# Optimization experiments

Hardware: AMD Instinct MI355X
Metric: run time of the kernel (lower is better)

## Reference

```python
import jax, jax.numpy as jnp
import numpy as np

D_MODEL = 512
N_HEADS = 8
MAX_DEPTH = 4
D_FF = 4 * D_MODEL
B, L = 4, 2048


def setup_inputs() -> dict:
    key = jax.random.key(0)
    ks = jax.random.split(key, 16)
    s = 0.02
    inp = {
        "x": jax.random.normal(ks[0], (B, L, D_MODEL), dtype=jnp.float32),
        # attention pre-norm
        "ln1_g": jnp.ones((D_MODEL,), jnp.float32),
        "ln1_b": jnp.zeros((D_MODEL,), jnp.float32),
        # MultiheadAttention in_proj (3D, D) and out_proj (D, D), torch (out, in) layout
        "Wqkv": jax.random.normal(ks[1], (3 * D_MODEL, D_MODEL), jnp.float32) * s,
        "bqkv": jnp.zeros((3 * D_MODEL,), jnp.float32),
        "Wo": jax.random.normal(ks[2], (D_MODEL, D_MODEL), jnp.float32) * s,
        "bo": jnp.zeros((D_MODEL,), jnp.float32),
        # FFN pre-norm + MLP
        "ln2_g": jnp.ones((D_MODEL,), jnp.float32),
        "ln2_b": jnp.zeros((D_MODEL,), jnp.float32),
        "W1": jax.random.normal(ks[3], (D_FF, D_MODEL), jnp.float32) * s,
        "b1": jnp.zeros((D_FF,), jnp.float32),
        "W2": jax.random.normal(ks[4], (D_MODEL, D_FF), jnp.float32) * s,
        "b2": jnp.zeros((D_MODEL,), jnp.float32),
        # token-choice depth router: LayerNorm + Linear(D,D) + GELU + Linear(D,max_depth)
        "rn_g": jnp.ones((D_MODEL,), jnp.float32),
        "rn_b": jnp.zeros((D_MODEL,), jnp.float32),
        "Rw1": jax.random.normal(ks[5], (D_MODEL, D_MODEL), jnp.float32) * s,
        "Rb1": jnp.zeros((D_MODEL,), jnp.float32),
        "Rw2": jax.random.normal(ks[6], (MAX_DEPTH, D_MODEL), jnp.float32) * s,
        "Rb2": jnp.zeros((MAX_DEPTH,), jnp.float32),
    }
    return inp


def _layernorm(x, g, b, eps=1e-5):
    mu = jnp.mean(x, axis=-1, keepdims=True)
    var = jnp.var(x, axis=-1, keepdims=True)
    return (x - mu) * jax.lax.rsqrt(var + eps) * g + b


def _block(x, ln1_g, ln1_b, Wqkv, bqkv, Wo, bo, ln2_g, ln2_b, W1, b1, W2, b2):
    Bb, Ll, D = x.shape
    H = N_HEADS
    dh = D // H
    # pre-norm self-attention
    h = _layernorm(x, ln1_g, ln1_b)
    qkv = h @ Wqkv.T + bqkv                      # (B, L, 3D)
    q, k, v = jnp.split(qkv, 3, axis=-1)
    q = q.reshape(Bb, Ll, H, dh)
    k = k.reshape(Bb, Ll, H, dh)
    v = v.reshape(Bb, Ll, H, dh)
    scores = jnp.einsum("blhd,bmhd->bhlm", q, k) / jnp.sqrt(jnp.float32(dh))
    attn = jax.nn.softmax(scores, axis=-1)
    o = jnp.einsum("bhlm,bmhd->blhd", attn, v).reshape(Bb, Ll, D)
    x = x + (o @ Wo.T + bo)
    # pre-norm FFN (exact-erf GELU, matching torch nn.GELU default)
    h2 = _layernorm(x, ln2_g, ln2_b)
    f = jax.nn.gelu(h2 @ W1.T + b1, approximate=False) @ W2.T + b2
    return x + f


def reference(x, ln1_g, ln1_b, Wqkv, bqkv, Wo, bo, ln2_g, ln2_b, W1, b1, W2, b2,
              rn_g, rn_b, Rw1, Rb1, Rw2, Rb2):
    # --- token-choice depth router (eval mode: argmax) ---
    rh = _layernorm(x, rn_g, rn_b)
    rh = jax.nn.gelu(rh @ Rw1.T + Rb1, approximate=False)
    router_logits = rh @ Rw2.T + Rb2             # (B, L, MAX_DEPTH)
    depths = jnp.argmax(router_logits, axis=-1) + 1  # (B, L) in [1, MAX_DEPTH]
    # --- dense recursion with torch.where-style selection ---
    cur = x
    for level in range(1, MAX_DEPTH + 1):
        upd = _block(cur, ln1_g, ln1_b, Wqkv, bqkv, Wo, bo,
                     ln2_g, ln2_b, W1, b1, W2, b2)
        keep = (depths >= level)[..., None]      # (B, L, 1)
        cur = jnp.where(keep, upd, cur)
    return cur, depths, router_logits
```

## Files before the change

kernel.cpp:

```cpp
#include <hip/hip_runtime.h>

typedef unsigned short u16;
typedef __attribute__((ext_vector_type(8))) short short8;
typedef __attribute__((ext_vector_type(4))) short s16x4;
typedef __attribute__((ext_vector_type(4))) float floatx4;
typedef __attribute__((ext_vector_type(4))) unsigned short u16x4;

#define NTOK 8192
#define DMODEL 512
#define DFF 2048
#define LSEQ 2048
#define RMARGIN 1e-3f

__device__ __forceinline__ u16 f2bf(float f) {
    union { float f; unsigned u; } x; x.f = f;
    unsigned r = (x.u + 0x7fffu + ((x.u >> 16) & 1u)) >> 16;
    return (u16)r;
}
__device__ __forceinline__ float bf2f(u16 h) {
    union { unsigned u; float f; } x; x.u = ((unsigned)h) << 16;
    return x.f;
}

__device__ __forceinline__ float geluf(float x) {
    return 0.5f * x * (1.0f + erff(x * 0.70710678118654752f));
}

__device__ __forceinline__ void gload_lds16(const void* g, void* l) {
    __builtin_amdgcn_global_load_lds(
        (const __attribute__((address_space(1))) void*)g,
        (__attribute__((address_space(3))) void*)l,
        16, 0, 0);
}

__device__ __forceinline__ s16x4 pack_p(float p0, float p1, float p2, float p3) {
    union { float f; unsigned u; } a{p0}, b{p1}, c{p2}, d{p3};
    union { unsigned u[2]; s16x4 s; } r;
    r.u[0] = (a.u >> 16) | (b.u & 0xffff0000u);
    r.u[1] = (c.u >> 16) | (d.u & 0xffff0000u);
    return r.s;
}

__global__ __launch_bounds__(256) void cvt_w(const float* __restrict__ wq,
                                             const float* __restrict__ wo,
                                             const float* __restrict__ w1,
                                             const float* __restrict__ w2,
                                             u16* __restrict__ out) {
    int i = blockIdx.x * 256 + threadIdx.x;
    float v;
    if (i < 786432)       v = wq[i];
    else if (i < 1048576) v = wo[i - 786432];
    else if (i < 2097152) v = w1[i - 1048576];
    else                  v = w2[i - 2097152];
    out[i] = f2bf(v);
}

__global__ __launch_bounds__(256) void copy_f32(const float* __restrict__ a,
                                                float* __restrict__ b) {
    size_t i = ((size_t)blockIdx.x * 256 + threadIdx.x) * 4;
    *(floatx4*)&b[i] = *(const floatx4*)&a[i];
}

__global__ __launch_bounds__(256) void cvt_rw1(const float* __restrict__ Rw1,
                                               u16* __restrict__ out) {
    const int i = blockIdx.x * 256 + threadIdx.x;
    const int n = i >> 9, k = i & 511;
    const float v = Rw1[i];
    const u16 hi = f2bf(v);
    const u16 lo = f2bf(v - bf2f(hi));
    out[(size_t)n * 1536 + k] = hi;
    out[(size_t)n * 1536 + 512 + k] = hi;
    out[(size_t)n * 1536 + 1024 + k] = lo;
}

__global__ __launch_bounds__(256) void cvt_split(const float* __restrict__ x,
                                                 u16* __restrict__ out,
                                                 int* __restrict__ cnt) {
    if (blockIdx.x == 0 && threadIdx.x == 0) *cnt = 0;
    const int i = blockIdx.x * 256 + threadIdx.x;
    const int base = i * 4;
    const int row = base >> 9, k = base & 511;
    const floatx4 v = *(const floatx4*)&x[base];
    u16x4 h, l;
#pragma unroll
    for (int e = 0; e < 4; ++e) {
        h[e] = f2bf(v[e]);
        l[e] = f2bf(v[e] - bf2f(h[e]));
    }
    u16* o = out + (size_t)row * 1536;
    *(u16x4*)&o[k] = h;
    *(u16x4*)&o[512 + k] = l;
    *(u16x4*)&o[1024 + k] = h;
}

__global__ __launch_bounds__(256)
void build_idx(const float* __restrict__ depthf, int* __restrict__ bcnt,
               int* __restrict__ idx) {
    __shared__ int sc[3][257];
    const int b = blockIdx.x;
    const int tid = threadIdx.x;
    const int t0 = (b << 11) + tid * 8;
    int dloc[8];
    int c2 = 0, c3 = 0, c4 = 0;
#pragma unroll
    for (int e = 0; e < 8; ++e) {
        dloc[e] = (int)depthf[t0 + e];
        c2 += (dloc[e] >= 2); c3 += (dloc[e] >= 3); c4 += (dloc[e] >= 4);
    }
    sc[0][tid + 1] = c2; sc[1][tid + 1] = c3; sc[2][tid + 1] = c4;
    if (tid == 0) { sc[0][0] = 0; sc[1][0] = 0; sc[2][0] = 0; }
    __syncthreads();
    for (int off = 1; off < 256; off <<= 1) {
        int v0 = 0, v1 = 0, v2 = 0;
        if (tid + 1 > off) {
            v0 = sc[0][tid + 1 - off];
            v1 = sc[1][tid + 1 - off];
            v2 = sc[2][tid + 1 - off];
        }
        __syncthreads();
        if (tid + 1 > off) {
            sc[0][tid + 1] += v0; sc[1][tid + 1] += v1; sc[2][tid + 1] += v2;
        }
        __syncthreads();
    }
    int p2 = sc[0][tid], p3 = sc[1][tid], p4 = sc[2][tid];
    const int seg = b << 11;
#pragma unroll
    for (int e = 0; e < 8; ++e) {
        const int t = t0 + e;
        idx[t] = t;
        if (dloc[e] >= 2) idx[8192 + seg + (p2++)] = t;
        if (dloc[e] >= 3) idx[16384 + seg + (p3++)] = t;
        if (dloc[e] >= 4) idx[24576 + seg + (p4++)] = t;
    }
    if (tid == 255) {
        bcnt[b]      = 2048;
        bcnt[4 + b]  = sc[0][256];
        bcnt[8 + b]  = sc[1][256];
        bcnt[12 + b] = sc[2][256];
    }
}

template<bool OUTF32, bool GATED>
__global__ __launch_bounds__(256)
void ln_k(const float* __restrict__ x, const float* __restrict__ g,
          const float* __restrict__ bb, void* __restrict__ outp,
          const int* __restrict__ bcnt) {
    const int row = blockIdx.x * 4 + (threadIdx.x >> 6);
    if (GATED) {
        if ((row & 2047) >= bcnt[row >> 11]) return;
    }
    const int lane = threadIdx.x & 63;
    const float* xr = x + (size_t)row * DMODEL;
    const int c0 = lane * 4, c1 = c0 + 256;
    floatx4 a = *(const floatx4*)&xr[c0];
    floatx4 b = *(const floatx4*)&xr[c1];
    float s = 0.f, sq = 0.f;
#pragma unroll
    for (int e = 0; e < 4; ++e) { s += a[e]; sq += a[e] * a[e]; }
#pragma unroll
    for (int e = 0; e < 4; ++e) { s += b[e]; sq += b[e] * b[e]; }
#pragma unroll
    for (int m = 32; m >= 1; m >>= 1) {
        s += __shfl_xor(s, m);
        sq += __shfl_xor(sq, m);
    }
    const float mean = s * (1.f / 512.f);
    const float rstd = rsqrtf(sq * (1.f / 512.f) - mean * mean + 1e-5f);
    floatx4 g0 = *(const floatx4*)&g[c0];
    floatx4 g1 = *(const floatx4*)&g[c1];
    floatx4 b0 = *(const floatx4*)&bb[c0];
    floatx4 b1 = *(const floatx4*)&bb[c1];
    floatx4 y0, y1;
#pragma unroll
    for (int e = 0; e < 4; ++e) {
        y0[e] = (a[e] - mean) * rstd * g0[e] + b0[e];
        y1[e] = (b[e] - mean) * rstd * g1[e] + b1[e];
    }
    if (OUTF32) {
        float* o = (float*)outp + (size_t)row * DMODEL;
        *(floatx4*)&o[c0] = y0;
        *(floatx4*)&o[c1] = y1;
    } else {
        u16* o = (u16*)outp + (size_t)row * DMODEL;
        u16x4 p0, p1;
#pragma unroll
        for (int e = 0; e < 4; ++e) { p0[e] = f2bf(y0[e]); p1[e] = f2bf(y1[e]); }
        *(u16x4*)&o[c0] = p0;
        *(u16x4*)&o[c1] = p1;
    }
}

template<int EPI, int BN>
__global__ __launch_bounds__(256, 2)
void gemm_bt(const u16* __restrict__ A, const u16* __restrict__ Bw,
             const float* __restrict__ bias,
             u16* __restrict__ Cb, float* __restrict__ Cf,
             const float* __restrict__ res,
             const int* __restrict__ IDX, const int* __restrict__ bcnt,
             u16* __restrict__ Cv,
             float aux, int N, int K) {
    constexpr int NJ = BN / 32;
    constexpr bool GATED = (EPI == 1 || EPI == 2 || EPI == 3);
    const int mBase = blockIdx.x * 128;
    int cntb = 0;
    if (GATED) {
        cntb = bcnt[mBase >> 11];
        if ((mBase & 2047) >= cntb) return;
    }
    __shared__ __align__(16) u16 As[128 * 32];
    __shared__ __align__(16) u16 Bs[BN * 32];
    const int tid = threadIdx.x;
    const int lane = tid & 63;
    const int w = tid >> 6;
    const int wm = (w >> 1) * 64;
    const int wn = (w & 1) * (BN / 2);
    const int nBase = blockIdx.y * BN;
    const int q4 = lane >> 4, rl = lane & 15;

    floatx4 acc[4][NJ];
#pragma unroll
    for (int i = 0; i < 4; ++i)
#pragma unroll
        for (int j = 0; j < NJ; ++j) acc[i][j] = (floatx4){0.f, 0.f, 0.f, 0.f};

    const int i0 = tid, i1 = tid + 256;
    const int ar0 = i0 >> 2, ac0 = ((i0 & 3) ^ ((i0 >> 3) & 3)) * 8;
    const int ar1 = i1 >> 2, ac1 = ((i1 & 3) ^ ((i1 >> 3) & 3)) * 8;
    const u16* pA0 = A + (size_t)(mBase + ar0) * K + ac0;
    const u16* pA1 = A + (size_t)(mBase + ar1) * K + ac1;
    const u16* pB0 = Bw + (size_t)(nBase + ar0) * K + ac0;
    const u16* pB1 = (BN == 128) ? Bw + (size_t)(nBase + ar1) * K + ac1 : pB0;
    u16* lA0 = &As[i0 * 8];
    u16* lA1 = &As[i1 * 8];
    u16* lB0 = &Bs[i0 * 8];
    u16* lB1 = (BN == 128) ? &Bs[i1 * 8] : lB0;

    for (int k0 = 0; k0 < K; k0 += 32) {
        gload_lds16(pA0, lA0);
        gload_lds16(pA1, lA1);
        gload_lds16(pB0, lB0);
        if (BN == 128) gload_lds16(pB1, lB1);
        pA0 += 32; pA1 += 32; pB0 += 32;
        if (BN == 128) pB1 += 32;
        __syncthreads();
        short8 af[4], bf[NJ];
#pragma unroll
        for (int t = 0; t < 4; ++t) {
            const int r = wm + t * 16 + rl;
            af[t] = *(const short8*)&As[r * 32 + (q4 ^ ((r >> 1) & 3)) * 8];
        }
#pragma unroll
        for (int t = 0; t < NJ; ++t) {
            const int r = wn + t * 16 + rl;
            bf[t] = *(const short8*)&Bs[r * 32 + (q4 ^ ((r >> 1) & 3)) * 8];
        }
#pragma unroll
        for (int ti = 0; ti < 4; ++ti)
#pragma unroll
            for (int tj = 0; tj < NJ; ++tj)
                acc[ti][tj] = __builtin_amdgcn_mfma_f32_16x16x32_bf16(
                    af[ti], bf[tj], acc[ti][tj], 0, 0, 0);
        __syncthreads();
    }

#pragma unroll
    for (int ti = 0; ti < 4; ++ti) {
        const int r0 = mBase + wm + ti * 16 + q4 * 4;
        int toks[4];
        if (EPI == 2 || EPI == 3) {
#pragma unroll
            for (int rr = 0; rr < 4; ++rr)
                toks[rr] = ((r0 + rr) & 2047) < cntb ? IDX[r0 + rr] : -1;
        }
#pragma unroll
        for (int tj = 0; tj < NJ; ++tj) {
            const int c = nBase + wn + tj * 16 + rl;
            const float bv = bias[c];
            if (EPI == 0) {
                if (nBase < 1024) {
                    const float sc = (nBase < 512) ? aux : 1.0f;
#pragma unroll
                    for (int rr = 0; rr < 4; ++rr)
                        Cb[(size_t)(r0 + rr) * 1024 + c] =
                            f2bf((acc[ti][tj][rr] + bv) * sc);
                } else {
                    const int cm = c - 1024;
                    const int hh = cm >> 6, dh = cm & 63;
                    const int bb2 = r0 >> 11, kv = r0 & 2047;
                    u16x4 pk;
#pragma unroll
                    for (int rr = 0; rr < 4; ++rr)
                        pk[rr] = f2bf(acc[ti][tj][rr] + bv);
                    *(u16x4*)&Cv[((size_t)(bb2 * 8 + hh) * 64 + dh) * 2048 + kv] = pk;
                }
            } else {
#pragma unroll
                for (int rr = 0; rr < 4; ++rr) {
                    const int r = r0 + rr;
                    const float v = acc[ti][tj][rr] + bv;
                    if (EPI == 1) {
                        Cb[(size_t)r * N + c] = f2bf(geluf(v));
                    } else if (EPI == 2) {
                        if (toks[rr] >= 0)
                            Cf[(size_t)r * N + c] =
                                res[(size_t)toks[rr] * N + c] + v;
                    } else if (EPI == 3) {
                        if (toks[rr] >= 0)
                            Cf[(size_t)toks[rr] * N + c] =
                                res[(size_t)r * N + c] + v;
                    } else {
                        Cf[(size_t)r * N + c] = geluf(v);
                    }
                }
            }
        }
    }
}

__global__ __launch_bounds__(256, 2)
void attn_k(const u16* __restrict__ qk, const u16* __restrict__ vT,
            u16* __restrict__ o, const int* __restrict__ IDX,
            const int* __restrict__ bcnt) {
    const int qt = blockIdx.x;
    const int bh = blockIdx.y;
    const int b = bh >> 3, h = bh & 7;
    const int cnt = bcnt[b];
    if (qt * 128 >= cnt) return;
    const int tid = threadIdx.x, lane = tid & 63, w = tid >> 6;
    const int tok0 = b * LSEQ;
    const int seg = b << 11;
    const int q4 = lane >> 4, rl = lane & 15;

    __shared__ __align__(16) u16 Kt[128 * 64];
    __shared__ __align__(16) u16 Vt[64 * 128];

    const u16* vbase = vT + (size_t)bh * 64 * 2048;

    const int pos0 = qt * 128 + w * 32 + rl;
    const int pos1 = pos0 + 16;
    const int tA = (pos0 < cnt) ? IDX[seg + pos0] : tok0;
    const int tB = (pos1 < cnt) ? IDX[seg + pos1] : tok0;

    short8 qf[2][2];
#pragma unroll
    for (int ks = 0; ks < 2; ++ks) {
        qf[0][ks] = *(const short8*)&qk[(size_t)tA * 1024 + h * 64 + ks * 32 + q4 * 8];
        qf[1][ks] = *(const short8*)&qk[(size_t)tB * 1024 + h * 64 + ks * 32 + q4 * 8];
    }

    floatx4 oacc[4][2];
#pragma unroll
    for (int dt = 0; dt < 4; ++dt)
#pragma unroll
        for (int nt = 0; nt < 2; ++nt) oacc[dt][nt] = (floatx4){0.f, 0.f, 0.f, 0.f};
    float lsum[2] = {0.f, 0.f};

    const u16* kp0 = &Kt[rl * 64 + ((q4 ^ (rl & 7))) * 8];
    const u16* kp1 = &Kt[rl * 64 + (((4 + q4) ^ (rl & 7))) * 8];

    for (int kt = 0; kt < 16; ++kt) {
        const int kv0 = kt * 128;
        __syncthreads();
#pragma unroll
        for (int it = 0; it < 4; ++it) {
            const int i = it * 256 + tid;
            const int r = i >> 3;
            const int c = ((i & 7) ^ (r & 7)) * 8;
            gload_lds16(&qk[(size_t)(tok0 + kv0 + r) * 1024 + 512 + h * 64 + c],
                        &Kt[i * 8]);
        }
#pragma unroll
        for (int it = 0; it < 4; ++it) {
            const int i = it * 256 + tid;
            const int dh = i >> 4;
            const int ch = (i & 15) ^ (dh & 15);
            gload_lds16(&vbase[(size_t)dh * 2048 + kv0 + ch * 8], &Vt[i * 8]);
        }
        __syncthreads();

#pragma unroll
        for (int mt = 0; mt < 8; ++mt) {
            const short8 kf0 = *(const short8*)&kp0[mt * 1024];
            const short8 kf1 = *(const short8*)&kp1[mt * 1024];
            floatx4 s[2];
#pragma unroll
            for (int nt = 0; nt < 2; ++nt) {
                s[nt] = __builtin_amdgcn_mfma_f32_16x16x32_bf16(kf0, qf[nt][0],
                        (floatx4){0.f, 0.f, 0.f, 0.f}, 0, 0, 0);
                s[nt] = __builtin_amdgcn_mfma_f32_16x16x32_bf16(kf1, qf[nt][1],
                        s[nt], 0, 0, 0);
            }
            s16x4 pb[2];
#pragma unroll
            for (int nt = 0; nt < 2; ++nt) {
                const float p0 = exp2f(s[nt][0]);
                const float p1 = exp2f(s[nt][1]);
                const float p2 = exp2f(s[nt][2]);
                const float p3 = exp2f(s[nt][3]);
                lsum[nt] += (p0 + p1) + (p2 + p3);
                pb[nt] = pack_p(p0, p1, p2, p3);
            }
            const int ct = 2 * mt + (q4 >> 1);
            const u16* vp = &Vt[(ct ^ rl) * 8 + (q4 & 1) * 4 + rl * 128];
#pragma unroll
            for (int dt = 0; dt < 4; ++dt) {
                const s16x4 vf = *(const s16x4*)&vp[dt * 2048];
#pragma unroll
                for (int nt = 0; nt < 2; ++nt)
                    oacc[dt][nt] = __builtin_amdgcn_mfma_f32_16x16x16bf16_1k(
                        vf, pb[nt], oacc[dt][nt], 0, 0, 0);
            }
        }
    }

#pragma unroll
    for (int nt = 0; nt < 2; ++nt) {
        float l = lsum[nt];
        l += __shfl_xor(l, 16);
        l += __shfl_xor(l, 32);
        const float inv = 1.0f / l;
        const int pos = (nt == 0) ? pos0 : pos1;
        if (pos < cnt) {
            const size_t row = seg + pos;
#pragma unroll
            for (int dt = 0; dt < 4; ++dt) {
                u16x4 pk;
#pragma unroll
                for (int rr = 0; rr < 4; ++rr) pk[rr] = f2bf(oacc[dt][nt][rr] * inv);
                *(u16x4*)&o[row * DMODEL + h * 64 + dt * 16 + q4 * 4] = pk;
            }
        }
    }
}

__global__ __launch_bounds__(256)
void router_logits_f32(const float* __restrict__ rr, const float* __restrict__ Rw2,
                       const float* __restrict__ Rb2, float* __restrict__ logits,
                       float* __restrict__ depthf, int* __restrict__ cnt,
                       int* __restrict__ list) {
    const int t = blockIdx.x * 4 + (threadIdx.x >> 6);
    const int lane = threadIdx.x & 63;
    const float* xr = rr + (size_t)t * 512;
    const int c0 = lane * 4, c1 = c0 + 256;
    floatx4 a = *(const floatx4*)&xr[c0];
    floatx4 b = *(const floatx4*)&xr[c1];
    float s[4];
#pragma unroll
    for (int d = 0; d < 4; ++d) {
        const float* wr = Rw2 + d * 512;
        floatx4 wa = *(const floatx4*)&wr[c0];
        floatx4 wb = *(const floatx4*)&wr[c1];
        float acc = 0.f;
#pragma unroll
        for (int e = 0; e < 4; ++e) acc += a[e] * wa[e];
#pragma unroll
        for (int e = 0; e < 4; ++e) acc += b[e] * wb[e];
        s[d] = acc;
    }
#pragma unroll
    for (int m = 32; m >= 1; m >>= 1)
#pragma unroll
        for (int d = 0; d < 4; ++d) s[d] += __shfl_xor(s[d], m);
    if (lane == 0) {
        float v[4];
        float bv = -1e30f; int best = 0;
#pragma unroll
        for (int d = 0; d < 4; ++d) {
            v[d] = s[d] + Rb2[d];
            logits[(size_t)t * 4 + d] = v[d];
            if (v[d] > bv) { bv = v[d]; best = d; }
        }
        float second = -1e30f;
#pragma unroll
        for (int d = 0; d < 4; ++d)
            if (d != best) second = fmaxf(second, v[d]);
        depthf[t] = (float)(best + 1);
        if (bv - second < RMARGIN) {
            int idx = atomicAdd(cnt, 1);
            list[idx] = t;
        }
    }
}

__global__ __launch_bounds__(256)
void router_exact(const float* __restrict__ rh, const float* __restrict__ Rw1,
                  const float* __restrict__ Rb1, const float* __restrict__ Rw2,
                  const float* __restrict__ Rb2, const int* __restrict__ cnt,
                  const int* __restrict__ list, float* __restrict__ logits,
                  float* __restrict__ depthf) {
    __shared__ float rhs[512];
    __shared__ double rrd[512];
    __shared__ double lg[4];
    const int n = *cnt;
    const int tid = threadIdx.x;
    for (int ii = blockIdx.x; ii < n; ii += gridDim.x) {
        const int t = list[ii];
        rhs[tid] = rh[(size_t)t * 512 + tid];
        rhs[tid + 256] = rh[(size_t)t * 512 + 256 + tid];
        __syncthreads();
#pragma unroll
        for (int oo = 0; oo < 2; ++oo) {
            const int nn = tid + oo * 256;
            double acc = (double)Rb1[nn];
            const float* wrow = Rw1 + (size_t)nn * 512;
            for (int k = 0; k < 512; ++k)
                acc = fma((double)rhs[k], (double)wrow[k], acc);
            rrd[nn] = 0.5 * acc * (1.0 + erf(acc * 0.70710678118654752440));
        }
        __syncthreads();
        const int w = tid >> 6, lane = tid & 63;
        double acc2 = 0.0;
        for (int k = lane; k < 512; k += 64)
            acc2 += rrd[k] * (double)Rw2[w * 512 + k];
#pragma unroll
        for (int m = 32; m >= 1; m >>= 1) acc2 += __shfl_xor(acc2, m);
        if (lane == 0) lg[w] = acc2 + (double)Rb2[w];
        __syncthreads();
        if (tid == 0) {
            double bv = -1e300; int best = 0;
#pragma unroll
            for (int d = 0; d < 4; ++d) {
                const double v = lg[d];
                logits[(size_t)t * 4 + d] = (float)v;
                if (v > bv) { bv = v; best = d; }
            }
            depthf[t] = (float)(best + 1);
        }
        __syncthreads();
    }
}

extern "C" void kernel_launch(void* const* d_in, const int* in_sizes, int n_in,
                              void* d_out, int out_size, void* d_ws, size_t ws_size,
                              hipStream_t stream) {
    (void)in_sizes; (void)n_in; (void)out_size; (void)ws_size;
    const float* x    = (const float*)d_in[0];
    const float* ln1g = (const float*)d_in[1];
    const float* ln1b = (const float*)d_in[2];
    const float* Wqkv = (const float*)d_in[3];
    const float* bqkv = (const float*)d_in[4];
    const float* Wo   = (const float*)d_in[5];
    const float* bo   = (const float*)d_in[6];
    const float* ln2g = (const float*)d_in[7];
    const float* ln2b = (const float*)d_in[8];
    const float* W1   = (const float*)d_in[9];
    const float* b1   = (const float*)d_in[10];
    const float* W2   = (const float*)d_in[11];
    const float* b2   = (const float*)d_in[12];
    const float* rng  = (const float*)d_in[13];
    const float* rnb  = (const float*)d_in[14];
    const float* Rw1  = (const float*)d_in[15];
    const float* Rb1  = (const float*)d_in[16];
    const float* Rw2  = (const float*)d_in[17];
    const float* Rb2  = (const float*)d_in[18];

    float* cur    = (float*)d_out;
    float* depthf = cur + (size_t)NTOK * DMODEL;
    float* logits = depthf + NTOK;

    char* ws = (char*)d_ws;
    float* xmid = (float*)ws;
    u16* sbuf   = (u16*)(ws + 16777216);
    u16* qk     = (u16*)(ws + 25165824);
    u16* ffb    = (u16*)(ws + 41943040);
    u16* vTb    = (u16*)(ws + 75497472);
    u16* wbf    = (u16*)(ws + 83886080);
    int* idxb   = (int*)(ws + 90177536);
    int* bcntb  = (int*)(ws + 90308608);

    u16* rw1s   = (u16*)(ws + 16777216);
    int* rcnt   = (int*)(ws + 18874368);
    int* rlist  = rcnt + 16;
    u16* asplit = ffb;
    float* rrf  = (float*)qk;

    u16* wq = wbf;
    u16* wo = wbf + 786432;
    u16* w1 = wbf + 1048576;
    u16* w2 = wbf + 2097152;

    const float qsc = 0.125f * 1.4426950408889634f;

    cvt_w<<<12288, 256, 0, stream>>>(Wqkv, Wo, W1, W2, wbf);
    copy_f32<<<4096, 256, 0, stream>>>(x, cur);

    ln_k<true, false><<<2048, 256, 0, stream>>>(x, rng, rnb, xmid, nullptr);
    cvt_rw1<<<1024, 256, 0, stream>>>(Rw1, rw1s);
    cvt_split<<<4096, 256, 0, stream>>>(xmid, asplit, rcnt);
    gemm_bt<4, 64><<<dim3(64, 8), 256, 0, stream>>>(
        asplit, rw1s, Rb1, nullptr, rrf, nullptr, nullptr, nullptr, nullptr,
        0.f, 512, 1536);
    router_logits_f32<<<2048, 256, 0, stream>>>(rrf, Rw2, Rb2, logits, depthf,
                                                rcnt, rlist);
    router_exact<<<128, 256, 0, stream>>>(xmid, Rw1, Rb1, Rw2, Rb2, rcnt, rlist,
                                          logits, depthf);
    build_idx<<<4, 256, 0, stream>>>(depthf, bcntb, idxb);

    for (int level = 1; level <= 4; ++level) {
        const int* IDXl = idxb + (level - 1) * 8192;
        const int* bcl  = bcntb + (level - 1) * 4;
        ln_k<false, false><<<2048, 256, 0, stream>>>(cur, ln1g, ln1b, sbuf, nullptr);
        gemm_bt<0, 128><<<dim3(64, 12), 256, 0, stream>>>(
            sbuf, wq, bqkv, qk, nullptr, nullptr, nullptr, nullptr, vTb,
            qsc, 1536, 512);
        attn_k<<<dim3(16, 32), 256, 0, stream>>>(qk, vTb, sbuf, IDXl, bcl);
        gemm_bt<2, 64><<<dim3(64, 8), 256, 0, stream>>>(
            sbuf, wo, bo, nullptr, xmid, cur, IDXl, bcl, nullptr, 0.f, 512, 512);
        ln_k<false, true><<<2048, 256, 0, stream>>>(xmid, ln2g, ln2b, sbuf, bcl);
        gemm_bt<1, 128><<<dim3(64, 16), 256, 0, stream>>>(
            sbuf, w1, b1, ffb, nullptr, nullptr, nullptr, bcl, nullptr,
            0.f, 2048, 512);
        gemm_bt<3, 64><<<dim3(64, 8), 256, 0, stream>>>(
            ffb, w2, b2, nullptr, cur, xmid, IDXl, bcl, nullptr,
            0.f, 512, 2048);
    }
}
```

Baseline: 950.1 us.

## Compute QKV only for tokens changed at previous level, scatter into persistent K/V

At levels two and up, the attention LayerNorm and QKV projection run only over tokens updated at the previous level, gathered via the previous level's index list. The QKV GEMM epilogue scatters results back by token id into the persistent Q/K and transposed V buffers, so unchanged tokens keep their earlier projections. The attention grid is also flattened and remapped so that consecutive blocks cover different batch-head pairs. This cuts redundant QKV work for tokens whose state did not change. In exchange it relies on stale buffers staying valid across levels and uses scalar scattered V stores where the rows are not contiguous.

```diff
diff --git a/kernel.cpp b/kernel.cpp
--- a/kernel.cpp
+++ b/kernel.cpp
@@ -141,17 +141,18 @@
     }
 }
 
-template<bool OUTF32, bool GATED>
+template<bool OUTF32, int MODE>
 __global__ __launch_bounds__(256)
 void ln_k(const float* __restrict__ x, const float* __restrict__ g,
           const float* __restrict__ bb, void* __restrict__ outp,
-          const int* __restrict__ bcnt) {
+          const int* __restrict__ bcnt, const int* __restrict__ IDX) {
     const int row = blockIdx.x * 4 + (threadIdx.x >> 6);
-    if (GATED) {
+    if (MODE != 0) {
         if ((row & 2047) >= bcnt[row >> 11]) return;
     }
+    const int src = (MODE == 2) ? IDX[row] : row;
     const int lane = threadIdx.x & 63;
-    const float* xr = x + (size_t)row * DMODEL;
+    const float* xr = x + (size_t)src * DMODEL;
     const int c0 = lane * 4, c1 = c0 + 256;
     floatx4 a = *(const floatx4*)&xr[c0];
     floatx4 b = *(const floatx4*)&xr[c1];
@@ -201,7 +202,7 @@
              u16* __restrict__ Cv,
              float aux, int N, int K) {
     constexpr int NJ = BN / 32;
-    constexpr bool GATED = (EPI == 1 || EPI == 2 || EPI == 3);
+    constexpr bool GATED = (EPI == 0 || EPI == 1 || EPI == 2 || EPI == 3);
     const int mBase = blockIdx.x * 128;
     int cntb = 0;
     if (GATED) {
@@ -268,7 +269,7 @@
     for (int ti = 0; ti < 4; ++ti) {
         const int r0 = mBase + wm + ti * 16 + q4 * 4;
         int toks[4];
-        if (EPI == 2 || EPI == 3) {
+        if (EPI == 0 || EPI == 2 || EPI == 3) {
 #pragma unroll
             for (int rr = 0; rr < 4; ++rr)
                 toks[rr] = ((r0 + rr) & 2047) < cntb ? IDX[r0 + rr] : -1;
@@ -282,17 +283,27 @@
                     const float sc = (nBase < 512) ? aux : 1.0f;
 #pragma unroll
                     for (int rr = 0; rr < 4; ++rr)
-                        Cb[(size_t)(r0 + rr) * 1024 + c] =
-                            f2bf((acc[ti][tj][rr] + bv) * sc);
+                        if (toks[rr] >= 0)
+                            Cb[(size_t)toks[rr] * 1024 + c] =
+                                f2bf((acc[ti][tj][rr] + bv) * sc);
                 } else {
                     const int cm = c - 1024;
                     const int hh = cm >> 6, dh = cm & 63;
-                    const int bb2 = r0 >> 11, kv = r0 & 2047;
-                    u16x4 pk;
+                    u16 pk[4];
 #pragma unroll
                     for (int rr = 0; rr < 4; ++rr)
                         pk[rr] = f2bf(acc[ti][tj][rr] + bv);
-                    *(u16x4*)&Cv[((size_t)(bb2 * 8 + hh) * 64 + dh) * 2048 + kv] = pk;
+                    if (toks[0] >= 0 && toks[3] == toks[0] + 3 && !(toks[0] & 3)) {
+                        u16x4 v4 = {pk[0], pk[1], pk[2], pk[3]};
+                        *(u16x4*)&Cv[((size_t)((toks[0] >> 11) * 8 + hh) * 64 + dh)
+                                     * 2048 + (toks[0] & 2047)] = v4;
+                    } else {
+#pragma unroll
+                        for (int rr = 0; rr < 4; ++rr)
+                            if (toks[rr] >= 0)
+                                Cv[((size_t)((toks[rr] >> 11) * 8 + hh) * 64 + dh)
+                                   * 2048 + (toks[rr] & 2047)] = pk[rr];
+                    }
                 }
             } else {
 #pragma unroll
@@ -322,8 +333,9 @@
 void attn_k(const u16* __restrict__ qk, const u16* __restrict__ vT,
             u16* __restrict__ o, const int* __restrict__ IDX,
             const int* __restrict__ bcnt) {
-    const int qt = blockIdx.x;
-    const int bh = blockIdx.y;
+    const int blk = blockIdx.x;
+    const int bh = ((blk & 7) << 2) | ((blk >> 3) & 3);
+    const int qt = blk >> 5;
     const int b = bh >> 3, h = bh & 7;
     const int cnt = bcnt[b];
     if (qt * 128 >= cnt) return;
@@ -585,7 +597,7 @@
     cvt_w<<<12288, 256, 0, stream>>>(Wqkv, Wo, W1, W2, wbf);
     copy_f32<<<4096, 256, 0, stream>>>(x, cur);
 
-    ln_k<true, false><<<2048, 256, 0, stream>>>(x, rng, rnb, xmid, nullptr);
+    ln_k<true, 0><<<2048, 256, 0, stream>>>(x, rng, rnb, xmid, nullptr, nullptr);
     cvt_rw1<<<1024, 256, 0, stream>>>(Rw1, rw1s);
     cvt_split<<<4096, 256, 0, stream>>>(xmid, asplit, rcnt);
     gemm_bt<4, 64><<<dim3(64, 8), 256, 0, stream>>>(
@@ -600,14 +612,23 @@
     for (int level = 1; level <= 4; ++level) {
         const int* IDXl = idxb + (level - 1) * 8192;
         const int* bcl  = bcntb + (level - 1) * 4;
-        ln_k<false, false><<<2048, 256, 0, stream>>>(cur, ln1g, ln1b, sbuf, nullptr);
+        const int pl = (level >= 2) ? (level - 2) : 0;
+        const int* IDXp = idxb + pl * 8192;
+        const int* bcp  = bcntb + pl * 4;
+        if (level == 1)
+            ln_k<false, 0><<<2048, 256, 0, stream>>>(cur, ln1g, ln1b, sbuf,
+                                                     nullptr, nullptr);
+        else
+            ln_k<false, 2><<<2048, 256, 0, stream>>>(cur, ln1g, ln1b, sbuf,
+                                                     bcp, IDXp);
         gemm_bt<0, 128><<<dim3(64, 12), 256, 0, stream>>>(
-            sbuf, wq, bqkv, qk, nullptr, nullptr, nullptr, nullptr, vTb,
+            sbuf, wq, bqkv, qk, nullptr, nullptr, IDXp, bcp, vTb,
             qsc, 1536, 512);
-        attn_k<<<dim3(16, 32), 256, 0, stream>>>(qk, vTb, sbuf, IDXl, bcl);
+        attn_k<<<512, 256, 0, stream>>>(qk, vTb, sbuf, IDXl, bcl);
         gemm_bt<2, 64><<<dim3(64, 8), 256, 0, stream>>>(
             sbuf, wo, bo, nullptr, xmid, cur, IDXl, bcl, nullptr, 0.f, 512, 512);
-        ln_k<false, true><<<2048, 256, 0, stream>>>(xmid, ln2g, ln2b, sbuf, bcl);
+        ln_k<false, 1><<<2048, 256, 0, stream>>>(xmid, ln2g, ln2b, sbuf,
+                                                 bcl, nullptr);
         gemm_bt<1, 128><<<dim3(64, 16), 256, 0, stream>>>(
             sbuf, w1, b1, ffb, nullptr, nullptr, nullptr, bcl, nullptr,
             0.f, 2048, 512);
```

Measured after the change: 943.7 us. About the same (-0.7%).
